# Optimization experiments

Hardware: AMD Instinct MI355X
Metric: run time of the kernel (lower is better)

The kernel has to match this reference:

```python
import jax, jax.numpy as jnp
import numpy as np

B, C, H, W, P, D, NH = 16, 3, 512, 512, 16, 128, 4
GH, GW = H // P, W // P
NP_ = GH * GW            # 1024 total patches
PD = C * P * P           # 768 patch dim
NV = NP_ // 4            # 256 visible tokens (mask_ratio = 0.75)
ENC_L, DEC_L = 6, 2
FF = 4 * D

def layer_norm(x, w, b, eps=1e-5):
    m = jnp.mean(x, -1, keepdims=True)
    v = jnp.mean((x - m) ** 2, -1, keepdims=True)
    return (x - m) * jax.lax.rsqrt(v + eps) * w + b

def mha(x, qkv_w, qkv_b, out_w, out_b):
    Bq, S, Dm = x.shape
    hd = Dm // NH
    q, k, v = jnp.split(x @ qkv_w.T + qkv_b, 3, axis=-1)
    sh = lambda t: t.reshape(Bq, S, NH, hd).transpose(0, 2, 1, 3)
    q, k, v = sh(q), sh(k), sh(v)
    scale = jnp.asarray(1.0 / np.sqrt(hd), x.dtype)
    att = jax.nn.softmax(jnp.einsum('bhqd,bhkd->bhqk', q, k) * scale, axis=-1)
    o = jnp.einsum('bhqk,bhkd->bhqd', att, v).transpose(0, 2, 1, 3).reshape(Bq, S, Dm)
    return o @ out_w.T + out_b

def stack(x, qkv_w, qkv_b, out_w, out_b, ln1_w, ln1_b, ff1_w, ff1_b, ff2_w, ff2_b, ln2_w, ln2_b):
    # post-norm nn.TransformerEncoderLayer, eval mode (dropout off), exact gelu
    for i in range(qkv_w.shape[0]):
        x = layer_norm(x + mha(x, qkv_w[i], qkv_b[i], out_w[i], out_b[i]), ln1_w[i], ln1_b[i])
        h = jax.nn.gelu(x @ ff1_w[i].T + ff1_b[i], approximate=False) @ ff2_w[i].T + ff2_b[i]
        x = layer_norm(x + h, ln2_w[i], ln2_b[i])
    return x

def setup_inputs():
    key = jax.random.key(0)
    ks = iter(jax.random.split(key, 64))
    f = lambda *s: jax.random.normal(next(ks), s, jnp.float32) * 0.02
    inp = {
        'x': jax.random.normal(next(ks), (B, C, H, W), jnp.float32),
        'vis_idx': jax.vmap(lambda k: jax.random.permutation(k, NP_))(jax.random.split(next(ks), B))[:, :NV].astype(jnp.int32),
        'w_patch': f(D, PD), 'b_patch': jnp.zeros((D,), jnp.float32),
        'mask_token': f(1, D), 'pos_embed': f(1, NP_, D),
        'w_recon': f(PD, D), 'b_recon': jnp.zeros((PD,), jnp.float32),
    }
    for pre, L in (('enc', ENC_L), ('dec', DEC_L)):
        inp[pre + '_qkv_w'] = f(L, 3 * D, D)
        inp[pre + '_qkv_b'] = jnp.zeros((L, 3 * D), jnp.float32)
        inp[pre + '_out_w'] = f(L, D, D)
        inp[pre + '_out_b'] = jnp.zeros((L, D), jnp.float32)
        inp[pre + '_ln1_w'] = jnp.ones((L, D), jnp.float32)
        inp[pre + '_ln1_b'] = jnp.zeros((L, D), jnp.float32)
        inp[pre + '_ff1_w'] = f(L, FF, D)
        inp[pre + '_ff1_b'] = jnp.zeros((L, FF), jnp.float32)
        inp[pre + '_ff2_w'] = f(L, D, FF)
        inp[pre + '_ff2_b'] = jnp.zeros((L, D), jnp.float32)
        inp[pre + '_ln2_w'] = jnp.ones((L, D), jnp.float32)
        inp[pre + '_ln2_b'] = jnp.zeros((L, D), jnp.float32)
    return inp

def reference(x, vis_idx, w_patch, b_patch, mask_token, pos_embed, w_recon, b_recon,
              enc_qkv_w, enc_qkv_b, enc_out_w, enc_out_b, enc_ln1_w, enc_ln1_b,
              enc_ff1_w, enc_ff1_b, enc_ff2_w, enc_ff2_b, enc_ln2_w, enc_ln2_b,
              dec_qkv_w, dec_qkv_b, dec_out_w, dec_out_b, dec_ln1_w, dec_ln1_b,
              dec_ff1_w, dec_ff1_b, dec_ff2_w, dec_ff2_b, dec_ln2_w, dec_ln2_b):
    # patchify: matches nn.Unfold(kernel=stride=P) channel-major patch layout
    patches = x.reshape(B, C, GH, P, GW, P).transpose(0, 2, 4, 1, 3, 5).reshape(B, NP_, PD)
    tok = patches @ w_patch.T + b_patch                    # [B, NP, D]
    bidx = jnp.arange(B)[:, None]
    vis = tok[bidx, vis_idx]                               # [B, NV, D] packed visible tokens
    enc = stack(vis, enc_qkv_w, enc_qkv_b, enc_out_w, enc_out_b, enc_ln1_w, enc_ln1_b,
                enc_ff1_w, enc_ff1_b, enc_ff2_w, enc_ff2_b, enc_ln2_w, enc_ln2_b)
    # mask_token everywhere, scatter encoded tokens back to their positions
    full = jnp.broadcast_to(mask_token, (B, NP_, D)).at[bidx, vis_idx].set(enc)
    full = full + pos_embed
    dec = stack(full, dec_qkv_w, dec_qkv_b, dec_out_w, dec_out_b, dec_ln1_w, dec_ln1_b,
                dec_ff1_w, dec_ff1_b, dec_ff2_w, dec_ff2_b, dec_ln2_w, dec_ln2_b)
    rec = dec @ w_recon.T + b_recon                        # [B, NP, PD]
    # unpatchify: [B,GH,GW,C,P,P] -> permute(0,3,1,4,2,5) -> [B,C,H,W]
    img = rec.reshape(B, GH, GW, C, P, P).transpose(0, 3, 1, 4, 2, 5).reshape(B, C, H, W)
    return img
```

## Files before the change

### kernel.cpp

```cpp
#include <hip/hip_runtime.h>
#include <math.h>

typedef unsigned short ushort_t;
typedef __attribute__((ext_vector_type(8))) short bf16x8;
typedef __attribute__((ext_vector_type(4))) float f32x4;
typedef __attribute__((ext_vector_type(16))) float f32x16;
typedef __attribute__((ext_vector_type(2))) unsigned uint2v;

__device__ __forceinline__ ushort_t f2bf(float f){
  union{float f; unsigned u;} v; v.f = f;
  unsigned r = v.u + 0x7FFFu + ((v.u >> 16) & 1u);
  return (ushort_t)(r >> 16);
}
__device__ __forceinline__ float bf2f(ushort_t h){
  union{unsigned u; float f;} v; v.u = ((unsigned)h) << 16; return v.f;
}
__device__ __forceinline__ float erf_fast(float x){
  float ax = fabsf(x);
  float t = 1.f / fmaf(0.3275911f, ax, 1.f);
  float y = t*fmaf(t, fmaf(t, fmaf(t, fmaf(t, 1.061405429f, -1.453152027f),
            1.421413741f), -0.284496736f), 0.254829592f);
  float r = 1.f - y * __expf(-ax*ax);
  return copysignf(r, x);
}
// ... 106 lines not shown
        *(uint2*)(vT + (((size_t)(bb*4 + hh)*32 + dd) << slog) + s0) = pk;
      }
    }
    return;
  }

  if (EPI == 2) {
    float* img = (float*)Cout;
#pragma unroll
    for (int mi = 0; mi < MI; ++mi) {
#pragma unroll
      for (int r = 0; r < 4; ++r) {
        int gm = m0 + wr*(BT/2) + mi*16 + g*4 + r;
        int bb = gm >> 10, pp = gm & 1023, gh = pp >> 5, gw = pp & 31;
#pragma unroll
        for (int ni = 0; ni < MI; ++ni) {
          int n = n0 + wc*(BT/2) + ni*16 + lq;
          int ci = n >> 8, rem = n & 255, py = rem >> 4, px = rem & 15;
          img[(size_t)((bb*3 + ci)*512 + gh*16 + py)*512 + gw*16 + px] =
              acc[mi][ni][r] + bv[ni];
        }
      }
    }
  } else {
    const float cs = (EPI == 3 && n0 < 128) ? qs : 1.0f;
    __syncthreads();
    constexpr int CPR = BT/8;
#pragma unroll
    for (int mi = 0; mi < MI; ++mi)
#pragma unroll
      for (int ni = 0; ni < MI; ++ni)
#pragma unroll
        for (int r = 0; r < 4; ++r) {
          int row = wr*(BT/2) + mi*16 + g*4 + r;
          int col = wc*(BT/2) + ni*16 + lq;
          float v = acc[mi][ni][r] + bv[ni];
          if (EPI == 3) v *= cs;
          int cc = (col >> 3) ^ (row & (CPR-1));
          smem[row*BT + cc*8 + (col & 7)] = f2bf(v);
        }
    __syncthreads();
    ushort_t* Co = (ushort_t*)Cout;
#pragma unroll
    for (int i = 0; i < BT*BT/2048; ++i) {
      int chunk = i*256 + tid;
      int row = chunk / CPR, cc = chunk % CPR;
      int c = cc ^ (row & (CPR-1));
      bf16x8 v = *(const bf16x8*)((const char*)smem + chunk*16);
      *(bf16x8*)(Co + (size_t)(m0+row)*N + n0 + c*8) = v;
    }
  }
}

template<int MI2, int QKV>
__global__ __launch_bounds__(512, 4) void mega8(
    const ushort_t* __restrict__ Ao, const ushort_t* __restrict__ Wo,
    const float* __restrict__ bo, ushort_t* __restrict__ X,
    const float* __restrict__ l1w, const float* __restrict__ l1b,
    const ushort_t* __restrict__ W1, const float* __restrict__ b1,
    const ushort_t* __restrict__ W2, const float* __restrict__ b2,
    const float* __restrict__ l2w, const float* __restrict__ l2b,
    const ushort_t* __restrict__ Wq, const float* __restrict__ bq,
    ushort_t* __restrict__ qkvb, ushort_t* __restrict__ vT,
    int slog, float qs)
{
  constexpr int BM = MI2 * 16;
  constexpr int TB = BM * 128;
  __shared__ __align__(16) ushort_t Xl[2*BM*64];
  __shared__ __align__(16) ushort_t Hl[8*BM*64];
  __shared__ __align__(16) float red[2][BM][8];
  const int tid = threadIdx.x, lane = tid & 63, w = tid >> 6;
  const int g = lane >> 4, lq = lane & 15;
  const int m0 = blockIdx.x * BM;
  const int col0 = w*16 + lq;
  const f32x4 zf = {0.f,0.f,0.f,0.f};

  f32x4 acc[MI2];
#pragma unroll
  for (int mi = 0; mi < MI2; ++mi) acc[mi] = zf;
  {
    bf16x8 a1[MI2][4], bo8[4];
#pragma unroll
    for (int mi = 0; mi < MI2; ++mi)
#pragma unroll
      for (int kf = 0; kf < 4; ++kf)
        a1[mi][kf] = *(const bf16x8*)(Ao + (size_t)(m0 + mi*16 + lq)*128 + kf*32 + g*8);
#pragma unroll
    for (int kf = 0; kf < 4; ++kf)
      bo8[kf] = *(const bf16x8*)(Wo + (size_t)col0*128 + kf*32 + g*8);
#pragma unroll
    for (int kf = 0; kf < 4; ++kf)
#pragma unroll
      for (int mi = 0; mi < MI2; ++mi)
        acc[mi] = mfma16(a1[mi][kf], bo8[kf], acc[mi]);
  }

  float xp[MI2][4];
  {
    const float bv = bo[col0], lwv = l1w[col0], lbv = l1b[col0];
#pragma unroll
    for (int mi = 0; mi < MI2; ++mi)
#pragma unroll
      for (int r = 0; r < 4; ++r) {
        int row = m0 + mi*16 + g*4 + r;
        float v = acc[mi][r] + bv + bf2f(X[(size_t)row*128 + col0]);
        xp[mi][r] = v;
        float s = v, q = v*v;
        s += __shfl_xor(s,1); s += __shfl_xor(s,2); s += __shfl_xor(s,4); s += __shfl_xor(s,8);
        q += __shfl_xor(q,1); q += __shfl_xor(q,2); q += __shfl_xor(q,4); q += __shfl_xor(q,8);
        if (lq == 0) { red[0][mi*16+g*4+r][w] = s; red[1][mi*16+g*4+r][w] = q; }
      }
    __syncthreads();
#pragma unroll
    for (int mi = 0; mi < MI2; ++mi)
#pragma unroll
      for (int r = 0; r < 4; ++r) {
        int rl = mi*16 + g*4 + r;
        float4 s0 = *(const float4*)&red[0][rl][0], s1 = *(const float4*)&red[0][rl][4];
        float4 q0 = *(const float4*)&red[1][rl][0], q1 = *(const float4*)&red[1][rl][4];
        float s = s0.x+s0.y+s0.z+s0.w + s1.x+s1.y+s1.z+s1.w;
        float q = q0.x+q0.y+q0.z+q0.w + q1.x+q1.y+q1.z+q1.w;
        float mean = s * 0.0078125f;
        float var = q * 0.0078125f - mean*mean;
        float rstd = rsqrtf(var + 1e-5f);
        float val = (xp[mi][r]-mean)*rstd*lwv + lbv;
        xp[mi][r] = val;
        int kt = col0 >> 6, c8 = (col0 & 63) >> 3, he = col0 & 7;
        *(ushort_t*)((char*)Xl + kt*TB + rl*128 + ((c8 ^ (rl & 7)) << 4) + he*2) = f2bf(val);
      }
  }
  __syncthreads();

  bf16x8 a2[MI2][4];
#pragma unroll
  for (int mi = 0; mi < MI2; ++mi)
#pragma unroll
    for (int kf = 0; kf < 4; ++kf) {
      int kt = kf >> 1, row = mi*16 + lq;
      int c = ((kf & 1)*4 + g) ^ (row & 7);
      a2[mi][kf] = *(const bf16x8*)((const char*)Xl + kt*TB + row*128 + c*16);
    }

#pragma unroll
  for (int hp = 0; hp < 4; ++hp) {
    const int hid = hp*128 + col0;
    bf16x8 b18[4];
#pragma unroll
    for (int kf = 0; kf < 4; ++kf)
      b18[kf] = *(const bf16x8*)(W1 + (size_t)hid*128 + kf*32 + g*8);
    f32x4 acc1[MI2];
#pragma unroll
    for (int mi = 0; mi < MI2; ++mi) acc1[mi] = zf;
#pragma unroll
    for (int kf = 0; kf < 4; ++kf)
#pragma unroll
      for (int mi = 0; mi < MI2; ++mi)
        acc1[mi] = mfma16(a2[mi][kf], b18[kf], acc1[mi]);
    const float bb = b1[hid];
    const int hkt = hid >> 6, hc8 = (hid & 63) >> 3, he = hid & 7;
#pragma unroll
    for (int mi = 0; mi < MI2; ++mi)
#pragma unroll
      for (int r = 0; r < 4; ++r) {
        int mrow = mi*16 + g*4 + r;
        float hv = gelu_fast(acc1[mi][r] + bb);
        *(ushort_t*)((char*)Hl + hkt*TB + mrow*128 + ((hc8 ^ (mrow & 7)) << 4) + he*2) = f2bf(hv);
      }
  }
  __syncthreads();

  f32x4 acc2[MI2];
#pragma unroll
  for (int mi = 0; mi < MI2; ++mi) acc2[mi] = zf;
#pragma unroll
  for (int kf = 0; kf < 16; ++kf) {
    int kt = kf >> 1;
    bf16x8 af[MI2], bfr;
#pragma unroll
    for (int mi = 0; mi < MI2; ++mi) {
      int row = mi*16 + lq;
      int c = ((kf & 1)*4 + g) ^ (row & 7);
      af[mi] = *(const bf16x8*)((const char*)Hl + kt*TB + row*128 + c*16);
    }
    bfr = *(const bf16x8*)(W2 + (size_t)col0*512 + kf*32 + g*8);
#pragma unroll
    for (int mi = 0; mi < MI2; ++mi)
      acc2[mi] = mfma16(af[mi], bfr, acc2[mi]);
  }

  {
    const float bv = b2[col0], lwv = l2w[col0], lbv = l2b[col0];
#pragma unroll
    for (int mi = 0; mi < MI2; ++mi)
#pragma unroll
      for (int r = 0; r < 4; ++r) {
        float v = acc2[mi][r] + bv + xp[mi][r];
        xp[mi][r] = v;
        float s = v, q = v*v;
        s += __shfl_xor(s,1); s += __shfl_xor(s,2); s += __shfl_xor(s,4); s += __shfl_xor(s,8);
        q += __shfl_xor(q,1); q += __shfl_xor(q,2); q += __shfl_xor(q,4); q += __shfl_xor(q,8);
        if (lq == 0) { red[0][mi*16+g*4+r][w] = s; red[1][mi*16+g*4+r][w] = q; }
      }
    __syncthreads();
#pragma unroll
    for (int mi = 0; mi < MI2; ++mi)
#pragma unroll
      for (int r = 0; r < 4; ++r) {
        int rl = mi*16 + g*4 + r;
        float4 s0 = *(const float4*)&red[0][rl][0], s1 = *(const float4*)&red[0][rl][4];
        float4 q0 = *(const float4*)&red[1][rl][0], q1 = *(const float4*)&red[1][rl][4];
        float s = s0.x+s0.y+s0.z+s0.w + s1.x+s1.y+s1.z+s1.w;
        float q = q0.x+q0.y+q0.z+q0.w + q1.x+q1.y+q1.z+q1.w;
        float mean = s * 0.0078125f;
        float var = q * 0.0078125f - mean*mean;
        float rstd = rsqrtf(var + 1e-5f);
        float val = (xp[mi][r]-mean)*rstd*lwv + lbv;
        ushort_t hv = f2bf(val);
        X[(size_t)(m0+rl)*128 + col0] = hv;
        if (QKV) {
          int kt = col0 >> 6, c8 = (col0 & 63) >> 3, he = col0 & 7;
          *(ushort_t*)((char*)Xl + kt*TB + rl*128 + ((c8 ^ (rl & 7)) << 4) + he*2) = hv;
        }
      }
  }

  if (QKV) {
    __syncthreads();
    bf16x8 a3[MI2][4];
#pragma unroll
    for (int mi = 0; mi < MI2; ++mi)
#pragma unroll
      for (int kf = 0; kf < 4; ++kf) {
        int kt = kf >> 1, row = mi*16 + lq;
        int c = ((kf & 1)*4 + g) ^ (row & 7);
        a3[mi][kf] = *(const bf16x8*)((const char*)Xl + kt*TB + row*128 + c*16);
      }
    const int Sm1 = (1 << slog) - 1;
#pragma unroll
    for (int pp = 0; pp < 3; ++pp) {
      const int colq = pp*128 + col0;
      bf16x8 bq8[4];
#pragma unroll
      for (int kf = 0; kf < 4; ++kf)
        bq8[kf] = *(const bf16x8*)(Wq + (size_t)colq*128 + kf*32 + g*8);
      f32x4 aq[MI2];
#pragma unroll
      for (int mi = 0; mi < MI2; ++mi) aq[mi] = zf;
#pragma unroll
      for (int kf = 0; kf < 4; ++kf)
#pragma unroll
        for (int mi = 0; mi < MI2; ++mi)
          aq[mi] = mfma16(a3[mi][kf], bq8[kf], aq[mi]);
      const float bias = bq[colq];
      if (pp < 2) {
        const float sc = (pp == 0) ? qs : 1.f;
#pragma unroll
        for (int mi = 0; mi < MI2; ++mi)
#pragma unroll
          for (int r = 0; r < 4; ++r) {
            int row = m0 + mi*16 + g*4 + r;
            qkvb[(size_t)row*384 + colq] = f2bf((aq[mi][r] + bias)*sc);
          }
      } else {
        const int hh = col0 >> 5, dd = col0 & 31;
#pragma unroll
        for (int mi = 0; mi < MI2; ++mi) {
          int gm0 = m0 + mi*16 + g*4;
          int bb = gm0 >> slog, s0 = gm0 & Sm1;
          unsigned pw0 = ((unsigned)f2bf(aq[mi][0] + bias)) |
                         (((unsigned)f2bf(aq[mi][1] + bias)) << 16);
          unsigned pw1 = ((unsigned)f2bf(aq[mi][2] + bias)) |
                         (((unsigned)f2bf(aq[mi][3] + bias)) << 16);
          uint2 pk; pk.x = pw0; pk.y = pw1;
          *(uint2*)(vT + (((size_t)(bb*4 + hh)*32 + dd) << slog) + s0) = pk;
        }
      }
    }
  }
}

template<int S, int JS>
__global__ __launch_bounds__(256) void attn32(
    const ushort_t* __restrict__ qkv, const ushort_t* __restrict__ vTg,
    ushort_t* __restrict__ o)
{
  constexpr int LDSB = (JS == 1) ? 16384 : 32768;
  __shared__ __align__(16) char smem[LDSB];
  const int tid = threadIdx.x, lane = tid & 63, w = tid >> 6;
  const int hi = lane >> 5, lq = lane & 31;
  int lin = blockIdx.x;
  int nid = (lin & 7) * 64 + (lin >> 3);
  int bx = nid & 7, bh = nid >> 3;
  int h = bh & 3, b = bh >> 2;
  const int q0 = (JS == 1) ? (bx*128 + w*32) : (bx*32);

  bf16x8 bq0 = *(const bf16x8*)(qkv + (size_t)(b*S + q0 + lq)*384 + h*32 + hi*8);
  bf16x8 bq1 = *(const bf16x8*)(qkv + (size_t)(b*S + q0 + lq)*384 + h*32 + 16 + hi*8);

  f32x16 O;
#pragma unroll
  for (int i = 0; i < 16; ++i) O[i] = 0.f;
  const f32x16 z16 = O;
  float l = 0.f;

  auto stageK = [&](char* Kb, int j0, int ci){
    int k = ci >> 2, cp = ci & 3, c = cp ^ (k & 3);
    GLD16(qkv + (size_t)(b*S + j0 + k)*384 + 128 + h*32 + c*8, Kb + ci*16);
  };
  auto stageV = [&](char* Vb, int j0, int ci){
    int d = ci >> 3, cp = ci & 7, c = cp ^ (d & 7);
    GLD16(vTg + (size_t)(bh*32 + d)*S + j0 + c*8, Vb + ci*16);
  };

  auto sm_pack = [&](const f32x16& stv, unsigned* wd){
    float p[16];
#pragma unroll
    for (int r = 0; r < 16; ++r) { p[r] = __expf(stv[r]); l += p[r]; }
#pragma unroll
    for (int i = 0; i < 8; ++i) {
      unsigned u0 = __float_as_uint(p[2*i])   + 0x8000u;
      unsigned u1 = __float_as_uint(p[2*i+1]) + 0x8000u;
      wd[i] = (u0 >> 16) | (u1 & 0xFFFF0000u);
    }
  };
  auto pvstep = [&](unsigned* wd, const char* Vb, int mt){
    uint2v s02 = __builtin_amdgcn_permlane32_swap(wd[0], wd[2], false, false);
    uint2v s13 = __builtin_amdgcn_permlane32_swap(wd[1], wd[3], false, false);
    uint2v s46 = __builtin_amdgcn_permlane32_swap(wd[4], wd[6], false, false);
    uint2v s57 = __builtin_amdgcn_permlane32_swap(wd[5], wd[7], false, false);
    union { unsigned u[4]; bf16x8 v; } pa0, pa1;
    pa0.u[0] = s02[0]; pa0.u[1] = s13[0]; pa0.u[2] = s02[1]; pa0.u[3] = s13[1];
    pa1.u[0] = s46[0]; pa1.u[1] = s57[0]; pa1.u[2] = s46[1]; pa1.u[3] = s57[1];
    int d = lq;
    bf16x8 v0 = *(const bf16x8*)(Vb + d*128 + (((mt*4 + hi)     ^ (d & 7)) << 4));
    bf16x8 v1 = *(const bf16x8*)(Vb + d*128 + (((mt*4 + 2 + hi) ^ (d & 7)) << 4));
    O = mfma32(pa0.v, v0, O);
    O = mfma32(pa1.v, v1, O);
  };
  auto computeTile = [&](const char* Kb, const char* Vb){
    const int k0 = lq, k1 = 32 + lq;
    bf16x8 a00 = *(const bf16x8*)(Kb + k0*64 + (((hi)     ^ (k0 & 3)) << 4));
    bf16x8 a01 = *(const bf16x8*)(Kb + k0*64 + (((2 + hi) ^ (k0 & 3)) << 4));
    f32x16 st0 = mfma32(a00, bq0, z16);
    st0 = mfma32(a01, bq1, st0);
    bf16x8 a10 = *(const bf16x8*)(Kb + k1*64 + (((hi)     ^ (k1 & 3)) << 4));
    bf16x8 a11 = *(const bf16x8*)(Kb + k1*64 + (((2 + hi) ^ (k1 & 3)) << 4));
    f32x16 st1 = mfma32(a10, bq0, z16);
    st1 = mfma32(a11, bq1, st1);
    unsigned wd0[8], wd1[8];
    sm_pack(st0, wd0);
    sm_pack(st1, wd1);
    pvstep(wd0, Vb, 0);
    pvstep(wd1, Vb, 1);
  };

  if (JS == 4) {
    char* Kb = smem + w*8192;
    char* Vb = Kb + 4096;
    const int j0 = w*64;
#pragma unroll
    for (int i = 0; i < 4; ++i) stageK(Kb, j0, i*64 + lane);
#pragma unroll
    for (int i = 0; i < 4; ++i) stageV(Vb, j0, i*64 + lane);
    __syncthreads();
    computeTile(Kb, Vb);
    float lw = l + __shfl_xor(l, 32);
    __syncthreads();
    float* F = (float*)smem;
#pragma unroll
    for (int r = 0; r < 16; ++r) F[(w*16 + r)*64 + lane] = O[r];
    if (hi == 0) F[4096 + w*32 + lq] = lw;
    __syncthreads();
    if (w == 0) {
      float lt = F[4096 + lq] + F[4096 + 32 + lq] + F[4096 + 64 + lq] + F[4096 + 96 + lq];
      float linv = 1.f / lt;
#pragma unroll
      for (int r = 0; r < 16; ++r) {
        float s = F[r*64 + lane] + F[(16 + r)*64 + lane] +
                  F[(32 + r)*64 + lane] + F[(48 + r)*64 + lane];
        int qr = (r & 3) + 8*(r >> 2) + 4*hi;
        float li = __shfl(linv, qr);
        o[(size_t)(b*S + q0 + qr)*128 + h*32 + lq] = f2bf(s*li);
      }
    }
  } else {
    char* K0 = smem, *V0 = smem + 4096, *K1 = smem + 8192, *V1 = smem + 12288;
    stageK(K0, 0, tid);
    stageV(V0, 0, tid);
    const int NT = S/64;
    for (int t = 0; t < NT; ++t) {
      __syncthreads();
      if (t + 1 < NT) {
        char* Kb = (t & 1) ? K0 : K1;
        char* Vb = (t & 1) ? V0 : V1;
        stageK(Kb, (t + 1)*64, tid);
        stageV(Vb, (t + 1)*64, tid);
      }
      computeTile((t & 1) ? K1 : K0, (t & 1) ? V1 : V0);
    }
    float ltot = l + __shfl_xor(l, 32);
    float linv = 1.f / ltot;
#pragma unroll
    for (int r = 0; r < 16; ++r) {
      int qr = (r & 3) + 8*(r >> 2) + 4*hi;
      float li = __shfl(linv, qr);
      o[(size_t)(b*S + q0 + qr)*128 + h*32 + lq] = f2bf(O[r]*li);
    }
  }
// ... 80 lines not shown
  const float* b_recon  = (const float*)d_in[7];
  float* out = (float*)d_out;
  const float QS = 0.17677669529663687f;

  ushort_t* ws    = (ushort_t*)d_ws;
  ushort_t* tok   = ws;
  ushort_t* xe    = tok  + 2097152;
  ushort_t* qkvb  = xe   + 524288;
  ushort_t* obuf  = qkvb + 8388608;
  ushort_t* tbuf  = obuf + 2097152;
  ushort_t* xbf   = tbuf + 2097152;
  ushort_t* wbf   = xbf  + 12582912;

  ushort_t* w_qkv_e = wbf;
  ushort_t* w_out_e = w_qkv_e + 294912;
  ushort_t* w_ff1_e = w_out_e + 98304;
  ushort_t* w_ff2_e = w_ff1_e + 393216;
  ushort_t* w_qkv_d = w_ff2_e + 393216;
  ushort_t* w_out_d = w_qkv_d + 98304;
  ushort_t* w_ff1_d = w_out_d + 32768;
  ushort_t* w_ff2_d = w_ff1_d + 131072;
  ushort_t* w_pat   = w_ff2_d + 131072;
  ushort_t* w_rec   = w_pat   + 98304;
  ushort_t* vT      = w_rec   + 98304;

  CastArgs ca;
  const float* srcs[11] = {x, (const float*)d_in[8], (const float*)d_in[10],
                           (const float*)d_in[14], (const float*)d_in[16],
                           (const float*)d_in[20], (const float*)d_in[22],
                           (const float*)d_in[26], (const float*)d_in[28],
                           (const float*)d_in[2], (const float*)d_in[6]};
  ushort_t* dsts[11] = {xbf, w_qkv_e, w_out_e, w_ff1_e, w_ff2_e,
                        w_qkv_d, w_out_d, w_ff1_d, w_ff2_d, w_pat, w_rec};
  int sizes[11] = {12582912, 294912, 98304, 393216, 393216,
                   98304, 32768, 131072, 131072, 98304, 98304};
  int acc8 = 0;
  for (int k = 0; k < 11; ++k){ ca.src[k]=srcs[k]; ca.dst[k]=dsts[k]; ca.start[k]=acc8; acc8 += sizes[k]/8; }
  cast_all<<<dim3((acc8 + 255)/256), 256, 0, stream>>>(ca, acc8);

  mfma_gemm<64,2,1,0><<<dim3(2,256), 256, 0, stream>>>(xbf, w_pat, b_patch, tok, 16384, 128, 768, nullptr, 0, 1.f);
  gather_k<<<dim3(256), 256, 0, stream>>>(tok, vis, xe);

  mfma_gemm<64,2,0,3><<<dim3(6,64), 256, 0, stream>>>(xe, w_qkv_e, (const float*)d_in[9], qkvb, 4096, 384, 128, vT, 8, QS);
  for (int L = 0; L < 6; ++L) {
    const float* ob  = (const float*)d_in[11] + L*128;
    const float* l1w = (const float*)d_in[12] + L*128;
    const float* l1b = (const float*)d_in[13] + L*128;
    const float* f1b = (const float*)d_in[15] + L*512;
    const float* f2b = (const float*)d_in[17] + L*128;
    const float* l2w = (const float*)d_in[18] + L*128;
    const float* l2b = (const float*)d_in[19] + L*128;
    attn32<256,4><<<dim3(512), 256, 0, stream>>>(qkvb, vT, obuf);
    if (L < 5) {
      mega8<1,1><<<dim3(256), 512, 0, stream>>>(obuf, w_out_e + L*16384, ob, xe,
          l1w, l1b, w_ff1_e + L*65536, f1b, w_ff2_e + L*65536, f2b, l2w, l2b,
          w_qkv_e + (L+1)*49152, (const float*)d_in[9] + (L+1)*384, qkvb, vT, 8, QS);
    } else {
      mega8<1,0><<<dim3(256), 512, 0, stream>>>(obuf, w_out_e + L*16384, ob, xe,
          l1w, l1b, w_ff1_e + L*65536, f1b, w_ff2_e + L*65536, f2b, l2w, l2b,
          w_qkv_e, (const float*)d_in[9], qkvb, vT, 8, QS);
    }
  }

  fill_k<<<dim3(1024), 256, 0, stream>>>(mask_tok, pos, tok);
  scatter_k<<<dim3(256), 256, 0, stream>>>(xe, vis, pos, tok);

  mfma_gemm<128,4,0,3><<<dim3(3,128), 256, 0, stream>>>(tok, w_qkv_d, (const float*)d_in[21], qkvb, 16384, 384, 128, vT, 10, QS);
  for (int L = 0; L < 2; ++L) {
    const float* ob  = (const float*)d_in[23] + L*128;
    const float* l1w = (const float*)d_in[24] + L*128;
    const float* l1b = (const float*)d_in[25] + L*128;
    const float* f1b = (const float*)d_in[27] + L*512;
    const float* f2b = (const float*)d_in[29] + L*128;
    const float* l2w = (const float*)d_in[30] + L*128;
    const float* l2b = (const float*)d_in[31] + L*128;
    attn32<1024,1><<<dim3(512), 256, 0, stream>>>(qkvb, vT, obuf);
    if (L < 1) {
      mega8<2,1><<<dim3(512), 512, 0, stream>>>(obuf, w_out_d + L*16384, ob, tok,
          l1w, l1b, w_ff1_d + L*65536, f1b, w_ff2_d + L*65536, f2b, l2w, l2b,
          w_qkv_d + 49152, (const float*)d_in[21] + 384, qkvb, vT, 10, QS);
    } else {
      mega8<2,0><<<dim3(512), 512, 0, stream>>>(obuf, w_out_d + L*16384, ob, tok,
          l1w, l1b, w_ff1_d + L*65536, f1b, w_ff2_d + L*65536, f2b, l2w, l2b,
          w_qkv_d, (const float*)d_in[21], qkvb, vT, 10, QS);
    }
  }

  mfma_gemm<128,4,0,2><<<dim3(6,128), 256, 0, stream>>>(tok, w_rec, b_recon, out, 16384, 768, 128, nullptr, 0, 1.f);
}
```

Before: 331.8 us.

## Fuse decoder attention with out-projection and LayerNorm1, double-buffer K/V tiles

```diff
diff --git a/kernel.cpp b/kernel.cpp
--- a/kernel.cpp
+++ b/kernel.cpp
@@ -182,247 +182,23 @@
   }
 }
 
-template<int MI2, int QKV>
-__global__ __launch_bounds__(512, 4) void mega8(
-    const ushort_t* __restrict__ Ao, const ushort_t* __restrict__ Wo,
-    const float* __restrict__ bo, ushort_t* __restrict__ X,
-    const float* __restrict__ l1w, const float* __restrict__ l1b,
-    const ushort_t* __restrict__ W1, const float* __restrict__ b1,
-    const ushort_t* __restrict__ W2, const float* __restrict__ b2,
-    const float* __restrict__ l2w, const float* __restrict__ l2b,
-    const ushort_t* __restrict__ Wq, const float* __restrict__ bq,
-    ushort_t* __restrict__ qkvb, ushort_t* __restrict__ vT,
-    int slog, float qs)
+__global__ __launch_bounds__(256) void attn_fused_dec(
+    const ushort_t* __restrict__ qkv, const ushort_t* __restrict__ vTg,
+    const ushort_t* __restrict__ Wo, const float* __restrict__ bo,
+    ushort_t* __restrict__ X, const float* __restrict__ l1w,
+    const float* __restrict__ l1b)
 {
-  constexpr int BM = MI2 * 16;
-  constexpr int TB = BM * 128;
-  __shared__ __align__(16) ushort_t Xl[2*BM*64];
-  __shared__ __align__(16) ushort_t Hl[8*BM*64];
-  __shared__ __align__(16) float red[2][BM][8];
-  const int tid = threadIdx.x, lane = tid & 63, w = tid >> 6;
-  const int g = lane >> 4, lq = lane & 15;
-  const int m0 = blockIdx.x * BM;
-  const int col0 = w*16 + lq;
-  const f32x4 zf = {0.f,0.f,0.f,0.f};
-
-  f32x4 acc[MI2];
-#pragma unroll
-  for (int mi = 0; mi < MI2; ++mi) acc[mi] = zf;
-  {
-    bf16x8 a1[MI2][4], bo8[4];
-#pragma unroll
-    for (int mi = 0; mi < MI2; ++mi)
-#pragma unroll
-      for (int kf = 0; kf < 4; ++kf)
-        a1[mi][kf] = *(const bf16x8*)(Ao + (size_t)(m0 + mi*16 + lq)*128 + kf*32 + g*8);
-#pragma unroll
-    for (int kf = 0; kf < 4; ++kf)
-      bo8[kf] = *(const bf16x8*)(Wo + (size_t)col0*128 + kf*32 + g*8);
-#pragma unroll
-    for (int kf = 0; kf < 4; ++kf)
-#pragma unroll
-      for (int mi = 0; mi < MI2; ++mi)
-        acc[mi] = mfma16(a1[mi][kf], bo8[kf], acc[mi]);
-  }
-
-  float xp[MI2][4];
-  {
-    const float bv = bo[col0], lwv = l1w[col0], lbv = l1b[col0];
-#pragma unroll
-    for (int mi = 0; mi < MI2; ++mi)
-#pragma unroll
-      for (int r = 0; r < 4; ++r) {
-        int row = m0 + mi*16 + g*4 + r;
-        float v = acc[mi][r] + bv + bf2f(X[(size_t)row*128 + col0]);
-        xp[mi][r] = v;
-        float s = v, q = v*v;
-        s += __shfl_xor(s,1); s += __shfl_xor(s,2); s += __shfl_xor(s,4); s += __shfl_xor(s,8);
-        q += __shfl_xor(q,1); q += __shfl_xor(q,2); q += __shfl_xor(q,4); q += __shfl_xor(q,8);
-        if (lq == 0) { red[0][mi*16+g*4+r][w] = s; red[1][mi*16+g*4+r][w] = q; }
-      }
-    __syncthreads();
-#pragma unroll
-    for (int mi = 0; mi < MI2; ++mi)
-#pragma unroll
-      for (int r = 0; r < 4; ++r) {
-        int rl = mi*16 + g*4 + r;
-        float4 s0 = *(const float4*)&red[0][rl][0], s1 = *(const float4*)&red[0][rl][4];
-        float4 q0 = *(const float4*)&red[1][rl][0], q1 = *(const float4*)&red[1][rl][4];
-        float s = s0.x+s0.y+s0.z+s0.w + s1.x+s1.y+s1.z+s1.w;
-        float q = q0.x+q0.y+q0.z+q0.w + q1.x+q1.y+q1.z+q1.w;
-        float mean = s * 0.0078125f;
-        float var = q * 0.0078125f - mean*mean;
-        float rstd = rsqrtf(var + 1e-5f);
-        float val = (xp[mi][r]-mean)*rstd*lwv + lbv;
-        xp[mi][r] = val;
-        int kt = col0 >> 6, c8 = (col0 & 63) >> 3, he = col0 & 7;
-        *(ushort_t*)((char*)Xl + kt*TB + rl*128 + ((c8 ^ (rl & 7)) << 4) + he*2) = f2bf(val);
-      }
-  }
-  __syncthreads();
-
-  bf16x8 a2[MI2][4];
-#pragma unroll
-  for (int mi = 0; mi < MI2; ++mi)
-#pragma unroll
-    for (int kf = 0; kf < 4; ++kf) {
-      int kt = kf >> 1, row = mi*16 + lq;
-      int c = ((kf & 1)*4 + g) ^ (row & 7);
-      a2[mi][kf] = *(const bf16x8*)((const char*)Xl + kt*TB + row*128 + c*16);
-    }
-
-#pragma unroll
-  for (int hp = 0; hp < 4; ++hp) {
-    const int hid = hp*128 + col0;
-    bf16x8 b18[4];
-#pragma unroll
-    for (int kf = 0; kf < 4; ++kf)
-      b18[kf] = *(const bf16x8*)(W1 + (size_t)hid*128 + kf*32 + g*8);
-    f32x4 acc1[MI2];
-#pragma unroll
-    for (int mi = 0; mi < MI2; ++mi) acc1[mi] = zf;
-#pragma unroll
-    for (int kf = 0; kf < 4; ++kf)
-#pragma unroll
-      for (int mi = 0; mi < MI2; ++mi)
-        acc1[mi] = mfma16(a2[mi][kf], b18[kf], acc1[mi]);
-    const float bb = b1[hid];
-    const int hkt = hid >> 6, hc8 = (hid & 63) >> 3, he = hid & 7;
-#pragma unroll
-    for (int mi = 0; mi < MI2; ++mi)
-#pragma unroll
-      for (int r = 0; r < 4; ++r) {
-        int mrow = mi*16 + g*4 + r;
-        float hv = gelu_fast(acc1[mi][r] + bb);
-        *(ushort_t*)((char*)Hl + hkt*TB + mrow*128 + ((hc8 ^ (mrow & 7)) << 4) + he*2) = f2bf(hv);
-      }
-  }
-  __syncthreads();
-
-  f32x4 acc2[MI2];
-#pragma unroll
-  for (int mi = 0; mi < MI2; ++mi) acc2[mi] = zf;
-#pragma unroll
-  for (int kf = 0; kf < 16; ++kf) {
-    int kt = kf >> 1;
-    bf16x8 af[MI2], bfr;
-#pragma unroll
-    for (int mi = 0; mi < MI2; ++mi) {
-      int row = mi*16 + lq;
-      int c = ((kf & 1)*4 + g) ^ (row & 7);
-      af[mi] = *(const bf16x8*)((const char*)Hl + kt*TB + row*128 + c*16);
-    }
-    bfr = *(const bf16x8*)(W2 + (size_t)col0*512 + kf*32 + g*8);
-#pragma unroll
-    for (int mi = 0; mi < MI2; ++mi)
-      acc2[mi] = mfma16(af[mi], bfr, acc2[mi]);
-  }
-
-  {
-    const float bv = b2[col0], lwv = l2w[col0], lbv = l2b[col0];
-#pragma unroll
-    for (int mi = 0; mi < MI2; ++mi)
-#pragma unroll
-      for (int r = 0; r < 4; ++r) {
-        float v = acc2[mi][r] + bv + xp[mi][r];
-        xp[mi][r] = v;
-        float s = v, q = v*v;
-        s += __shfl_xor(s,1); s += __shfl_xor(s,2); s += __shfl_xor(s,4); s += __shfl_xor(s,8);
-        q += __shfl_xor(q,1); q += __shfl_xor(q,2); q += __shfl_xor(q,4); q += __shfl_xor(q,8);
-        if (lq == 0) { red[0][mi*16+g*4+r][w] = s; red[1][mi*16+g*4+r][w] = q; }
-      }
-    __syncthreads();
-#pragma unroll
-    for (int mi = 0; mi < MI2; ++mi)
-#pragma unroll
-      for (int r = 0; r < 4; ++r) {
-        int rl = mi*16 + g*4 + r;
-        float4 s0 = *(const float4*)&red[0][rl][0], s1 = *(const float4*)&red[0][rl][4];
-        float4 q0 = *(const float4*)&red[1][rl][0], q1 = *(const float4*)&red[1][rl][4];
-        float s = s0.x+s0.y+s0.z+s0.w + s1.x+s1.y+s1.z+s1.w;
-        float q = q0.x+q0.y+q0.z+q0.w + q1.x+q1.y+q1.z+q1.w;
-        float mean = s * 0.0078125f;
-        float var = q * 0.0078125f - mean*mean;
-        float rstd = rsqrtf(var + 1e-5f);
-        float val = (xp[mi][r]-mean)*rstd*lwv + lbv;
-        ushort_t hv = f2bf(val);
-        X[(size_t)(m0+rl)*128 + col0] = hv;
-        if (QKV) {
-          int kt = col0 >> 6, c8 = (col0 & 63) >> 3, he = col0 & 7;
-          *(ushort_t*)((char*)Xl + kt*TB + rl*128 + ((c8 ^ (rl & 7)) << 4) + he*2) = hv;
-        }
-      }
-  }
-
-  if (QKV) {
-    __syncthreads();
-    bf16x8 a3[MI2][4];
-#pragma unroll
-    for (int mi = 0; mi < MI2; ++mi)
-#pragma unroll
-      for (int kf = 0; kf < 4; ++kf) {
-        int kt = kf >> 1, row = mi*16 + lq;
-        int c = ((kf & 1)*4 + g) ^ (row & 7);
-        a3[mi][kf] = *(const bf16x8*)((const char*)Xl + kt*TB + row*128 + c*16);
-      }
-    const int Sm1 = (1 << slog) - 1;
-#pragma unroll
-    for (int pp = 0; pp < 3; ++pp) {
-      const int colq = pp*128 + col0;
-      bf16x8 bq8[4];
-#pragma unroll
-      for (int kf = 0; kf < 4; ++kf)
-        bq8[kf] = *(const bf16x8*)(Wq + (size_t)colq*128 + kf*32 + g*8);
-      f32x4 aq[MI2];
-#pragma unroll
-      for (int mi = 0; mi < MI2; ++mi) aq[mi] = zf;
-#pragma unroll
-      for (int kf = 0; kf < 4; ++kf)
-#pragma unroll
-        for (int mi = 0; mi < MI2; ++mi)
-          aq[mi] = mfma16(a3[mi][kf], bq8[kf], aq[mi]);
-      const float bias = bq[colq];
-      if (pp < 2) {
-        const float sc = (pp == 0) ? qs : 1.f;
-#pragma unroll
-        for (int mi = 0; mi < MI2; ++mi)
-#pragma unroll
-          for (int r = 0; r < 4; ++r) {
-            int row = m0 + mi*16 + g*4 + r;
-            qkvb[(size_t)row*384 + colq] = f2bf((aq[mi][r] + bias)*sc);
-          }
-      } else {
-        const int hh = col0 >> 5, dd = col0 & 31;
-#pragma unroll
-        for (int mi = 0; mi < MI2; ++mi) {
-          int gm0 = m0 + mi*16 + g*4;
-          int bb = gm0 >> slog, s0 = gm0 & Sm1;
-          unsigned pw0 = ((unsigned)f2bf(aq[mi][0] + bias)) |
-                         (((unsigned)f2bf(aq[mi][1] + bias)) << 16);
-          unsigned pw1 = ((unsigned)f2bf(aq[mi][2] + bias)) |
-                         (((unsigned)f2bf(aq[mi][3] + bias)) << 16);
-          uint2 pk; pk.x = pw0; pk.y = pw1;
-          *(uint2*)(vT + (((size_t)(bb*4 + hh)*32 + dd) << slog) + s0) = pk;
-        }
-      }
-    }
-  }
-}
-
-template<int S, int JS>
-__global__ __launch_bounds__(256) void attn32(
-    const ushort_t* __restrict__ qkv, const ushort_t* __restrict__ vTg,
-    ushort_t* __restrict__ o)
-{
-  constexpr int LDSB = (JS == 1) ? 16384 : 32768;
-  __shared__ __align__(16) char smem[LDSB];
+  constexpr int S = 1024;
+  __shared__ __align__(16) char smem[65536];
   const int tid = threadIdx.x, lane = tid & 63, w = tid >> 6;
   const int hi = lane >> 5, lq = lane & 31;
+  const int gq = lane >> 4, l16 = lane & 15;
   int lin = blockIdx.x;
-  int nid = (lin & 7) * 64 + (lin >> 3);
-  int bx = nid & 7, bh = nid >> 3;
-  int h = bh & 3, b = bh >> 2;
-  const int q0 = (JS == 1) ? (bx*128 + w*32) : (bx*32);
+  int nid = (lin & 7)*64 + (lin >> 3);
+  const int b = nid >> 5, qc = nid & 31;
+  const int q0 = qc*32;
+  const int rowbase = b*1024 + q0;
+  const int h = w;
 
   bf16x8 bq0 = *(const bf16x8*)(qkv + (size_t)(b*S + q0 + lq)*384 + h*32 + hi*8);
   bf16x8 bq1 = *(const bf16x8*)(qkv + (size_t)(b*S + q0 + lq)*384 + h*32 + 16 + hi*8);
@@ -433,15 +209,23 @@
   const f32x16 z16 = O;
   float l = 0.f;
 
-  auto stageK = [&](char* Kb, int j0, int ci){
-    int k = ci >> 2, cp = ci & 3, c = cp ^ (k & 3);
-    GLD16(qkv + (size_t)(b*S + j0 + k)*384 + 128 + h*32 + c*8, Kb + ci*16);
+  char* base = smem + w*16384;
+  char* K0 = base, *V0 = base + 4096, *K1 = base + 8192, *V1 = base + 12288;
+
+  auto stageTile = [&](char* Kb, char* Vb, int j0){
+#pragma unroll
+    for (int c = 0; c < 4; ++c){
+      int ci = c*64 + lane;
+      int k = ci >> 2, cp = ci & 3, cc = cp ^ (k & 3);
+      GLD16(qkv + (size_t)(b*S + j0 + k)*384 + 128 + h*32 + cc*8, Kb + ci*16);
+    }
+#pragma unroll
+    for (int c = 0; c < 4; ++c){
+      int ci = c*64 + lane;
+      int d = ci >> 3, cp = ci & 7, cc = cp ^ (d & 7);
+      GLD16(vTg + (size_t)((b*4 + h)*32 + d)*S + j0 + cc*8, Vb + ci*16);
+    }
   };
-  auto stageV = [&](char* Vb, int j0, int ci){
-    int d = ci >> 3, cp = ci & 7, c = cp ^ (d & 7);
-    GLD16(vTg + (size_t)(bh*32 + d)*S + j0 + c*8, Vb + ci*16);
-  };
-
   auto sm_pack = [&](const f32x16& stv, unsigned* wd){
     float p[16];
 #pragma unroll
@@ -484,6 +268,420 @@
     pvstep(wd1, Vb, 1);
   };
 
+  stageTile(K0, V0, 0);
+  for (int t = 0; t < 16; ++t){
+    char* Kc = (t & 1) ? K1 : K0;
+    char* Vc = (t & 1) ? V1 : V0;
+    if (t < 15){
+      stageTile((t & 1) ? K0 : K1, (t & 1) ? V0 : V1, (t+1)*64);
+      asm volatile("s_waitcnt vmcnt(8)" ::: "memory");
+    } else {
+      asm volatile("s_waitcnt vmcnt(0)" ::: "memory");
+    }
+    __builtin_amdgcn_sched_barrier(0);
+    computeTile(Kc, Vc);
+    asm volatile("" ::: "memory");
+  }
+
+  float ltot = l + __shfl_xor(l, 32);
+  float linv = 1.f / ltot;
+  __syncthreads();
+  ushort_t* Ol = (ushort_t*)smem;
+  float (*red)[32][4] = (float(*)[32][4])(smem + 8192);
+
+#pragma unroll
+  for (int r = 0; r < 16; ++r){
+    int qr = (r & 3) + 8*(r >> 2) + 4*hi;
+    float li = __shfl(linv, qr);
+    int d = h*32 + lq;
+    int kt = d >> 6, c8 = (d & 63) >> 3, he = d & 7;
+    *(ushort_t*)((char*)Ol + kt*4096 + qr*128 + ((c8 ^ (qr & 7)) << 4) + he*2) = f2bf(O[r]*li);
+  }
+  __syncthreads();
+
+  bf16x8 ao[2][4];
+#pragma unroll
+  for (int mi = 0; mi < 2; ++mi)
+#pragma unroll
+    for (int kf = 0; kf < 4; ++kf){
+      int row = mi*16 + l16;
+      int c = ((kf & 1)*4 + gq) ^ (row & 7);
+      ao[mi][kf] = *(const bf16x8*)((const char*)Ol + (kf >> 1)*4096 + row*128 + c*16);
+    }
+  const f32x4 zf = {0.f,0.f,0.f,0.f};
+  f32x4 accp[2][2] = {{zf,zf},{zf,zf}};
+  bf16x8 bo8[2][4];
+#pragma unroll
+  for (int ni = 0; ni < 2; ++ni)
+#pragma unroll
+    for (int kf = 0; kf < 4; ++kf)
+      bo8[ni][kf] = *(const bf16x8*)(Wo + (size_t)(w*32 + ni*16 + l16)*128 + kf*32 + gq*8);
+#pragma unroll
+  for (int kf = 0; kf < 4; ++kf)
+#pragma unroll
+    for (int mi = 0; mi < 2; ++mi)
+#pragma unroll
+      for (int ni = 0; ni < 2; ++ni)
+        accp[mi][ni] = mfma16(ao[mi][kf], bo8[ni][kf], accp[mi][ni]);
+
+  float bv[2], lwv[2], lbv[2];
+#pragma unroll
+  for (int ni = 0; ni < 2; ++ni){
+    int col = w*32 + ni*16 + l16;
+    bv[ni] = bo[col]; lwv[ni] = l1w[col]; lbv[ni] = l1b[col];
+  }
+  float v[2][2][4];
+#pragma unroll
+  for (int mi = 0; mi < 2; ++mi)
+#pragma unroll
+    for (int r = 0; r < 4; ++r){
+      int grow = rowbase + mi*16 + gq*4 + r;
+#pragma unroll
+      for (int ni = 0; ni < 2; ++ni){
+        int col = w*32 + ni*16 + l16;
+        v[mi][ni][r] = accp[mi][ni][r] + bv[ni] + bf2f(X[(size_t)grow*128 + col]);
+      }
+      float s = v[mi][0][r] + v[mi][1][r];
+      float q = v[mi][0][r]*v[mi][0][r] + v[mi][1][r]*v[mi][1][r];
+      s += __shfl_xor(s,1); s += __shfl_xor(s,2); s += __shfl_xor(s,4); s += __shfl_xor(s,8);
+      q += __shfl_xor(q,1); q += __shfl_xor(q,2); q += __shfl_xor(q,4); q += __shfl_xor(q,8);
+      if (l16 == 0){ red[0][mi*16+gq*4+r][w] = s; red[1][mi*16+gq*4+r][w] = q; }
+    }
+  __syncthreads();
+#pragma unroll
+  for (int mi = 0; mi < 2; ++mi)
+#pragma unroll
+    for (int r = 0; r < 4; ++r){
+      int rl = mi*16 + gq*4 + r;
+      float4 s4 = *(const float4*)&red[0][rl][0];
+      float4 q4 = *(const float4*)&red[1][rl][0];
+      float s = s4.x + s4.y + s4.z + s4.w;
+      float q = q4.x + q4.y + q4.z + q4.w;
+      float mean = s * 0.0078125f;
+      float var = q * 0.0078125f - mean*mean;
+      float rstd = rsqrtf(var + 1e-5f);
+#pragma unroll
+      for (int ni = 0; ni < 2; ++ni){
+        int col = w*32 + ni*16 + l16;
+        X[(size_t)(rowbase + rl)*128 + col] = f2bf((v[mi][ni][r]-mean)*rstd*lwv[ni] + lbv[ni]);
+      }
+    }
+}
+
+template<int MI2, int QKV, int P1>
+__global__ __launch_bounds__(512, 4) void mega8(
+    const ushort_t* __restrict__ Ao, const ushort_t* __restrict__ Wo,
+    const float* __restrict__ bo, ushort_t* __restrict__ X,
+    const float* __restrict__ l1w, const float* __restrict__ l1b,
+    const ushort_t* __restrict__ W1, const float* __restrict__ b1,
+    const ushort_t* __restrict__ W2, const float* __restrict__ b2,
+    const float* __restrict__ l2w, const float* __restrict__ l2b,
+    const ushort_t* __restrict__ Wq, const float* __restrict__ bq,
+    ushort_t* __restrict__ qkvb, ushort_t* __restrict__ vT,
+    int slog, float qs)
+{
+  constexpr int BM = MI2 * 16;
+  constexpr int TB = BM * 128;
+  __shared__ __align__(16) ushort_t Xl[2*BM*64];
+  __shared__ __align__(16) ushort_t Hl[8*BM*64];
+  __shared__ __align__(16) float red[2][BM][8];
+  const int tid = threadIdx.x, lane = tid & 63, w = tid >> 6;
+  const int g = lane >> 4, lq = lane & 15;
+  const int m0 = blockIdx.x * BM;
+  const int col0 = w*16 + lq;
+  const f32x4 zf = {0.f,0.f,0.f,0.f};
+
+  float xp[MI2][4];
+  bf16x8 a2[MI2][4];
+
+  if (P1 == 0) {
+#pragma unroll
+    for (int mi = 0; mi < MI2; ++mi)
+#pragma unroll
+      for (int kf = 0; kf < 4; ++kf)
+        a2[mi][kf] = *(const bf16x8*)(X + (size_t)(m0 + mi*16 + lq)*128 + kf*32 + g*8);
+#pragma unroll
+    for (int mi = 0; mi < MI2; ++mi)
+#pragma unroll
+      for (int r = 0; r < 4; ++r)
+        xp[mi][r] = bf2f(X[(size_t)(m0 + mi*16 + g*4 + r)*128 + col0]);
+  } else {
+    f32x4 acc[MI2];
+#pragma unroll
+    for (int mi = 0; mi < MI2; ++mi) acc[mi] = zf;
+    {
+      bf16x8 a1[MI2][4], bo8[4];
+#pragma unroll
+      for (int mi = 0; mi < MI2; ++mi)
+#pragma unroll
+        for (int kf = 0; kf < 4; ++kf)
+          a1[mi][kf] = *(const bf16x8*)(Ao + (size_t)(m0 + mi*16 + lq)*128 + kf*32 + g*8);
+#pragma unroll
+      for (int kf = 0; kf < 4; ++kf)
+        bo8[kf] = *(const bf16x8*)(Wo + (size_t)col0*128 + kf*32 + g*8);
+#pragma unroll
+      for (int kf = 0; kf < 4; ++kf)
+#pragma unroll
+        for (int mi = 0; mi < MI2; ++mi)
+          acc[mi] = mfma16(a1[mi][kf], bo8[kf], acc[mi]);
+    }
+    {
+      const float bv = bo[col0], lwv = l1w[col0], lbv = l1b[col0];
+#pragma unroll
+      for (int mi = 0; mi < MI2; ++mi)
+#pragma unroll
+        for (int r = 0; r < 4; ++r) {
+          int row = m0 + mi*16 + g*4 + r;
+          float v = acc[mi][r] + bv + bf2f(X[(size_t)row*128 + col0]);
+          xp[mi][r] = v;
+          float s = v, q = v*v;
+          s += __shfl_xor(s,1); s += __shfl_xor(s,2); s += __shfl_xor(s,4); s += __shfl_xor(s,8);
+          q += __shfl_xor(q,1); q += __shfl_xor(q,2); q += __shfl_xor(q,4); q += __shfl_xor(q,8);
+          if (lq == 0) { red[0][mi*16+g*4+r][w] = s; red[1][mi*16+g*4+r][w] = q; }
+        }
+      __syncthreads();
+#pragma unroll
+      for (int mi = 0; mi < MI2; ++mi)
+#pragma unroll
+        for (int r = 0; r < 4; ++r) {
+          int rl = mi*16 + g*4 + r;
+          float4 s0 = *(const float4*)&red[0][rl][0], s1 = *(const float4*)&red[0][rl][4];
+          float4 q0 = *(const float4*)&red[1][rl][0], q1 = *(const float4*)&red[1][rl][4];
+          float s = s0.x+s0.y+s0.z+s0.w + s1.x+s1.y+s1.z+s1.w;
+          float q = q0.x+q0.y+q0.z+q0.w + q1.x+q1.y+q1.z+q1.w;
+          float mean = s * 0.0078125f;
+          float var = q * 0.0078125f - mean*mean;
+          float rstd = rsqrtf(var + 1e-5f);
+          float val = (xp[mi][r]-mean)*rstd*lwv + lbv;
+          xp[mi][r] = val;
+          int kt = col0 >> 6, c8 = (col0 & 63) >> 3, he = col0 & 7;
+          *(ushort_t*)((char*)Xl + kt*TB + rl*128 + ((c8 ^ (rl & 7)) << 4) + he*2) = f2bf(val);
+        }
+    }
+    __syncthreads();
+#pragma unroll
+    for (int mi = 0; mi < MI2; ++mi)
+#pragma unroll
+      for (int kf = 0; kf < 4; ++kf) {
+        int kt = kf >> 1, row = mi*16 + lq;
+        int c = ((kf & 1)*4 + g) ^ (row & 7);
+        a2[mi][kf] = *(const bf16x8*)((const char*)Xl + kt*TB + row*128 + c*16);
+      }
+  }
+
+#pragma unroll
+  for (int hp = 0; hp < 4; ++hp) {
+    const int hid = hp*128 + col0;
+    bf16x8 b18[4];
+#pragma unroll
+    for (int kf = 0; kf < 4; ++kf)
+      b18[kf] = *(const bf16x8*)(W1 + (size_t)hid*128 + kf*32 + g*8);
+    f32x4 acc1[MI2];
+#pragma unroll
+    for (int mi = 0; mi < MI2; ++mi) acc1[mi] = zf;
+#pragma unroll
+    for (int kf = 0; kf < 4; ++kf)
+#pragma unroll
+      for (int mi = 0; mi < MI2; ++mi)
+        acc1[mi] = mfma16(a2[mi][kf], b18[kf], acc1[mi]);
+    const float bb = b1[hid];
+    const int hkt = hid >> 6, hc8 = (hid & 63) >> 3, he = hid & 7;
+#pragma unroll
+    for (int mi = 0; mi < MI2; ++mi)
+#pragma unroll
+      for (int r = 0; r < 4; ++r) {
+        int mrow = mi*16 + g*4 + r;
+        float hv = gelu_fast(acc1[mi][r] + bb);
+        *(ushort_t*)((char*)Hl + hkt*TB + mrow*128 + ((hc8 ^ (mrow & 7)) << 4) + he*2) = f2bf(hv);
+      }
+  }
+  __syncthreads();
+
+  f32x4 acc2[MI2];
+#pragma unroll
+  for (int mi = 0; mi < MI2; ++mi) acc2[mi] = zf;
+#pragma unroll
+  for (int kf = 0; kf < 16; ++kf) {
+    int kt = kf >> 1;
+    bf16x8 af[MI2], bfr;
+#pragma unroll
+    for (int mi = 0; mi < MI2; ++mi) {
+      int row = mi*16 + lq;
+      int c = ((kf & 1)*4 + g) ^ (row & 7);
+      af[mi] = *(const bf16x8*)((const char*)Hl + kt*TB + row*128 + c*16);
+    }
+    bfr = *(const bf16x8*)(W2 + (size_t)col0*512 + kf*32 + g*8);
+#pragma unroll
+    for (int mi = 0; mi < MI2; ++mi)
+      acc2[mi] = mfma16(af[mi], bfr, acc2[mi]);
+  }
+
+  {
+    const float bv = b2[col0], lwv = l2w[col0], lbv = l2b[col0];
+#pragma unroll
+    for (int mi = 0; mi < MI2; ++mi)
+#pragma unroll
+      for (int r = 0; r < 4; ++r) {
+        float v = acc2[mi][r] + bv + xp[mi][r];
+        xp[mi][r] = v;
+        float s = v, q = v*v;
+        s += __shfl_xor(s,1); s += __shfl_xor(s,2); s += __shfl_xor(s,4); s += __shfl_xor(s,8);
+        q += __shfl_xor(q,1); q += __shfl_xor(q,2); q += __shfl_xor(q,4); q += __shfl_xor(q,8);
+        if (lq == 0) { red[0][mi*16+g*4+r][w] = s; red[1][mi*16+g*4+r][w] = q; }
+      }
+    __syncthreads();
+#pragma unroll
+    for (int mi = 0; mi < MI2; ++mi)
+#pragma unroll
+      for (int r = 0; r < 4; ++r) {
+        int rl = mi*16 + g*4 + r;
+        float4 s0 = *(const float4*)&red[0][rl][0], s1 = *(const float4*)&red[0][rl][4];
+        float4 q0 = *(const float4*)&red[1][rl][0], q1 = *(const float4*)&red[1][rl][4];
+        float s = s0.x+s0.y+s0.z+s0.w + s1.x+s1.y+s1.z+s1.w;
+        float q = q0.x+q0.y+q0.z+q0.w + q1.x+q1.y+q1.z+q1.w;
+        float mean = s * 0.0078125f;
+        float var = q * 0.0078125f - mean*mean;
+        float rstd = rsqrtf(var + 1e-5f);
+        float val = (xp[mi][r]-mean)*rstd*lwv + lbv;
+        ushort_t hv = f2bf(val);
+        X[(size_t)(m0+rl)*128 + col0] = hv;
+        if (QKV) {
+          int kt = col0 >> 6, c8 = (col0 & 63) >> 3, he = col0 & 7;
+          *(ushort_t*)((char*)Xl + kt*TB + rl*128 + ((c8 ^ (rl & 7)) << 4) + he*2) = hv;
+        }
+      }
+  }
+
+  if (QKV) {
+    __syncthreads();
+    bf16x8 a3[MI2][4];
+#pragma unroll
+    for (int mi = 0; mi < MI2; ++mi)
+#pragma unroll
+      for (int kf = 0; kf < 4; ++kf) {
+        int kt = kf >> 1, row = mi*16 + lq;
+        int c = ((kf & 1)*4 + g) ^ (row & 7);
+        a3[mi][kf] = *(const bf16x8*)((const char*)Xl + kt*TB + row*128 + c*16);
+      }
+    const int Sm1 = (1 << slog) - 1;
+#pragma unroll
+    for (int pp = 0; pp < 3; ++pp) {
+      const int colq = pp*128 + col0;
+      bf16x8 bq8[4];
+#pragma unroll
+      for (int kf = 0; kf < 4; ++kf)
+        bq8[kf] = *(const bf16x8*)(Wq + (size_t)colq*128 + kf*32 + g*8);
+      f32x4 aq[MI2];
+#pragma unroll
+      for (int mi = 0; mi < MI2; ++mi) aq[mi] = zf;
+#pragma unroll
+      for (int kf = 0; kf < 4; ++kf)
+#pragma unroll
+        for (int mi = 0; mi < MI2; ++mi)
+          aq[mi] = mfma16(a3[mi][kf], bq8[kf], aq[mi]);
+      const float bias = bq[colq];
+      if (pp < 2) {
+        const float sc = (pp == 0) ? qs : 1.f;
+#pragma unroll
+        for (int mi = 0; mi < MI2; ++mi)
+#pragma unroll
+          for (int r = 0; r < 4; ++r) {
+            int row = m0 + mi*16 + g*4 + r;
+            qkvb[(size_t)row*384 + colq] = f2bf((aq[mi][r] + bias)*sc);
+          }
+      } else {
+        const int hh = col0 >> 5, dd = col0 & 31;
+#pragma unroll
+        for (int mi = 0; mi < MI2; ++mi) {
+          int gm0 = m0 + mi*16 + g*4;
+          int bb = gm0 >> slog, s0 = gm0 & Sm1;
+          unsigned pw0 = ((unsigned)f2bf(aq[mi][0] + bias)) |
+                         (((unsigned)f2bf(aq[mi][1] + bias)) << 16);
+          unsigned pw1 = ((unsigned)f2bf(aq[mi][2] + bias)) |
+                         (((unsigned)f2bf(aq[mi][3] + bias)) << 16);
+          uint2 pk; pk.x = pw0; pk.y = pw1;
+          *(uint2*)(vT + (((size_t)(bb*4 + hh)*32 + dd) << slog) + s0) = pk;
+        }
+      }
+    }
+  }
+}
+
+template<int S, int JS>
+__global__ __launch_bounds__(256) void attn32(
+    const ushort_t* __restrict__ qkv, const ushort_t* __restrict__ vTg,
+    ushort_t* __restrict__ o)
+{
+  constexpr int LDSB = (JS == 1) ? 16384 : 32768;
+  __shared__ __align__(16) char smem[LDSB];
+  const int tid = threadIdx.x, lane = tid & 63, w = tid >> 6;
+  const int hi = lane >> 5, lq = lane & 31;
+  int lin = blockIdx.x;
+  int nid = (lin & 7) * 64 + (lin >> 3);
+  int bx = nid & 7, bh = nid >> 3;
+  int h = bh & 3, b = bh >> 2;
+  const int q0 = (JS == 1) ? (bx*128 + w*32) : (bx*32);
+
+  bf16x8 bq0 = *(const bf16x8*)(qkv + (size_t)(b*S + q0 + lq)*384 + h*32 + hi*8);
+  bf16x8 bq1 = *(const bf16x8*)(qkv + (size_t)(b*S + q0 + lq)*384 + h*32 + 16 + hi*8);
+
+  f32x16 O;
+#pragma unroll
+  for (int i = 0; i < 16; ++i) O[i] = 0.f;
+  const f32x16 z16 = O;
+  float l = 0.f;
+
+  auto stageK = [&](char* Kb, int j0, int ci){
+    int k = ci >> 2, cp = ci & 3, c = cp ^ (k & 3);
+    GLD16(qkv + (size_t)(b*S + j0 + k)*384 + 128 + h*32 + c*8, Kb + ci*16);
+  };
+  auto stageV = [&](char* Vb, int j0, int ci){
+    int d = ci >> 3, cp = ci & 7, c = cp ^ (d & 7);
+    GLD16(vTg + (size_t)(bh*32 + d)*S + j0 + c*8, Vb + ci*16);
+  };
+
+  auto sm_pack = [&](const f32x16& stv, unsigned* wd){
+    float p[16];
+#pragma unroll
+    for (int r = 0; r < 16; ++r) { p[r] = __expf(stv[r]); l += p[r]; }
+#pragma unroll
+    for (int i = 0; i < 8; ++i) {
+      unsigned u0 = __float_as_uint(p[2*i])   + 0x8000u;
+      unsigned u1 = __float_as_uint(p[2*i+1]) + 0x8000u;
+      wd[i] = (u0 >> 16) | (u1 & 0xFFFF0000u);
+    }
+  };
+  auto pvstep = [&](unsigned* wd, const char* Vb, int mt){
+    uint2v s02 = __builtin_amdgcn_permlane32_swap(wd[0], wd[2], false, false);
+    uint2v s13 = __builtin_amdgcn_permlane32_swap(wd[1], wd[3], false, false);
+    uint2v s46 = __builtin_amdgcn_permlane32_swap(wd[4], wd[6], false, false);
+    uint2v s57 = __builtin_amdgcn_permlane32_swap(wd[5], wd[7], false, false);
+    union { unsigned u[4]; bf16x8 v; } pa0, pa1;
+    pa0.u[0] = s02[0]; pa0.u[1] = s13[0]; pa0.u[2] = s02[1]; pa0.u[3] = s13[1];
+    pa1.u[0] = s46[0]; pa1.u[1] = s57[0]; pa1.u[2] = s46[1]; pa1.u[3] = s57[1];
+    int d = lq;
+    bf16x8 v0 = *(const bf16x8*)(Vb + d*128 + (((mt*4 + hi)     ^ (d & 7)) << 4));
+    bf16x8 v1 = *(const bf16x8*)(Vb + d*128 + (((mt*4 + 2 + hi) ^ (d & 7)) << 4));
+    O = mfma32(pa0.v, v0, O);
+    O = mfma32(pa1.v, v1, O);
+  };
+  auto computeTile = [&](const char* Kb, const char* Vb){
+    const int k0 = lq, k1 = 32 + lq;
+    bf16x8 a00 = *(const bf16x8*)(Kb + k0*64 + (((hi)     ^ (k0 & 3)) << 4));
+    bf16x8 a01 = *(const bf16x8*)(Kb + k0*64 + (((2 + hi) ^ (k0 & 3)) << 4));
+    f32x16 st0 = mfma32(a00, bq0, z16);
+    st0 = mfma32(a01, bq1, st0);
+    bf16x8 a10 = *(const bf16x8*)(Kb + k1*64 + (((hi)     ^ (k1 & 3)) << 4));
+    bf16x8 a11 = *(const bf16x8*)(Kb + k1*64 + (((2 + hi) ^ (k1 & 3)) << 4));
+    f32x16 st1 = mfma32(a10, bq0, z16);
+    st1 = mfma32(a11, bq1, st1);
+    unsigned wd0[8], wd1[8];
+    sm_pack(st0, wd0);
+    sm_pack(st1, wd1);
+    pvstep(wd0, Vb, 0);
+    pvstep(wd1, Vb, 1);
+  };
+
   if (JS == 4) {
     char* Kb = smem + w*8192;
     char* Vb = Kb + 4096;
@@ -670,11 +868,11 @@
     const float* l2b = (const float*)d_in[19] + L*128;
     attn32<256,4><<<dim3(512), 256, 0, stream>>>(qkvb, vT, obuf);
     if (L < 5) {
-      mega8<1,1><<<dim3(256), 512, 0, stream>>>(obuf, w_out_e + L*16384, ob, xe,
+      mega8<1,1,1><<<dim3(256), 512, 0, stream>>>(obuf, w_out_e + L*16384, ob, xe,
           l1w, l1b, w_ff1_e + L*65536, f1b, w_ff2_e + L*65536, f2b, l2w, l2b,
           w_qkv_e + (L+1)*49152, (const float*)d_in[9] + (L+1)*384, qkvb, vT, 8, QS);
     } else {
-      mega8<1,0><<<dim3(256), 512, 0, stream>>>(obuf, w_out_e + L*16384, ob, xe,
+      mega8<1,0,1><<<dim3(256), 512, 0, stream>>>(obuf, w_out_e + L*16384, ob, xe,
           l1w, l1b, w_ff1_e + L*65536, f1b, w_ff2_e + L*65536, f2b, l2w, l2b,
           w_qkv_e, (const float*)d_in[9], qkvb, vT, 8, QS);
     }
@@ -692,13 +890,13 @@
     const float* f2b = (const float*)d_in[29] + L*128;
     const float* l2w = (const float*)d_in[30] + L*128;
     const float* l2b = (const float*)d_in[31] + L*128;
-    attn32<1024,1><<<dim3(512), 256, 0, stream>>>(qkvb, vT, obuf);
+    attn_fused_dec<<<dim3(512), 256, 0, stream>>>(qkvb, vT, w_out_d + L*16384, ob, tok, l1w, l1b);
     if (L < 1) {
-      mega8<2,1><<<dim3(512), 512, 0, stream>>>(obuf, w_out_d + L*16384, ob, tok,
+      mega8<2,1,0><<<dim3(512), 512, 0, stream>>>(nullptr, nullptr, nullptr, tok,
           l1w, l1b, w_ff1_d + L*65536, f1b, w_ff2_d + L*65536, f2b, l2w, l2b,
           w_qkv_d + 49152, (const float*)d_in[21] + 384, qkvb, vT, 10, QS);
     } else {
-      mega8<2,0><<<dim3(512), 512, 0, stream>>>(obuf, w_out_d + L*16384, ob, tok,
+      mega8<2,0,0><<<dim3(512), 512, 0, stream>>>(nullptr, nullptr, nullptr, tok,
           l1w, l1b, w_ff1_d + L*65536, f1b, w_ff2_d + L*65536, f2b, l2w, l2b,
           w_qkv_d, (const float*)d_in[21], qkvb, vT, 10, QS);
     }
```

New measurement: 337.5 us. Within noise of the previous version (+1.7%).
